# Optimization experiments

Measured on AMD Instinct MI355X. Metric: run time of the kernel, lower is better.

## Reference

```python
import jax, jax.numpy as jnp
import numpy as np

MAX_ITERS = 20
TOL = 1e-6
STEP = 1.0
EPS = 1e-7
CLIP = 1e-7


def _normalize(x, axis=-1):
    n = jnp.linalg.norm(x, axis=axis, keepdims=True)
    return x / jnp.maximum(n, 1e-12)


def _safe_acos(x):
    return jnp.arccos(jnp.clip(x, -1.0 + CLIP, 1.0 - CLIP))


def setup_inputs() -> dict:
    key = jax.random.key(0)
    NC, K, N, D = 1000, 8, 32, 128
    X_groups = jax.random.normal(key, (NC, K, N, D), dtype=jnp.float32)
    return {"X_groups": X_groups}


def reference(X_groups):
    # X_groups: (NC, K, N, D)
    NC, K, N, D = X_groups.shape
    X = X_groups.reshape(NC * K, N, D)
    Xn = _normalize(X)                      # (G, N, D) unit vectors
    mu = _normalize(jnp.mean(Xn, axis=1))   # (G, D) init mean

    done = jnp.array(False)
    for _ in range(MAX_ITERS):
        dots = jnp.einsum('gd,gnd->gn', mu, Xn)             # (G, N)
        theta = _safe_acos(dots)
        sin_t = jnp.maximum(jnp.sin(theta), EPS)
        diff = Xn - dots[..., None] * mu[:, None, :]        # (G, N, D)
        log_vecs = (theta / sin_t)[..., None] * diff        # log map
        v = jnp.mean(log_vecs, axis=1)                      # (G, D)
        v_norm = jnp.maximum(jnp.linalg.norm(v, axis=-1, keepdims=True), EPS)
        done = done | (jnp.max(v_norm) < TOL)               # global convergence (as in torch .item() check)
        v_step = STEP * v
        vs_norm = jnp.maximum(jnp.linalg.norm(v_step, axis=-1, keepdims=True), EPS)
        mu_new = jnp.cos(vs_norm) * mu + jnp.sin(vs_norm) * (v_step / vs_norm)  # exp map
        mu_new = _normalize(mu_new)
        mu = jnp.where(done, mu, mu_new)

    # calc_cluster_distance: features (G, N, D) @ means (G, D)
    sims = jnp.einsum('gnd,gd->gn', Xn, mu)
    sims = jnp.clip(sims, -1 + CLIP, 1 - CLIP)
    loss = jnp.mean(jnp.sum(jnp.arccos(sims) ** 2, axis=-1))
    return loss
```

## Files before the change

### kernel.cpp

```cpp
#include <hip/hip_runtime.h>
#include <stdint.h>

#define MAX_ITERS 20
#define EPSV 1e-7f
#define CLIPV 1e-7f
#define PI_F 3.14159265358979f
#define PIO2_F 1.57079632679490f

typedef __attribute__((ext_vector_type(8))) short short8;
typedef __attribute__((ext_vector_type(4))) float f4;

__device__ __forceinline__ f4 mfma_bf16(short8 a, short8 b, f4 c) {
    return __builtin_amdgcn_mfma_f32_16x16x32_bf16(a, b, c, 0, 0, 0);
}

__device__ __forceinline__ float rl(float v, int l) {
    return __int_as_float(__builtin_amdgcn_readlane(__float_as_int(v), l));
}

template <int CTRL>
__device__ __forceinline__ float dpp_add(float v) {
    int p = __builtin_amdgcn_update_dpp(0, __float_as_int(v), CTRL, 0xF, 0xF, true);
    return v + __int_as_float(p);
}
template <int CTRL>
__device__ __forceinline__ float dpp_mov(float v) {
    return __int_as_float(__builtin_amdgcn_update_dpp(0, __float_as_int(v), CTRL, 0xF, 0xF, true));
}

__device__ __forceinline__ float rowsum16(float v) {
    v = dpp_add<0xB1>(v);
    v = dpp_add<0x4E>(v);
    v = dpp_add<0x141>(v);
    v = dpp_add<0x140>(v);
    return v;
}

__device__ __forceinline__ float halfsum_rl(float v, bool hB) {
    v = rowsum16(v);
    float sA = rl(v, 0) + rl(v, 16);
    float sB = rl(v, 32) + rl(v, 48);
    return hB ? sB : sA;
}

__device__ __forceinline__ float halfsum_sw(float v) {
    v = rowsum16(v);
    int sw = __builtin_amdgcn_ds_swizzle(__float_as_int(v), 0x401F);
    return v + __int_as_float(sw);
}

__device__ __forceinline__ float fast_acos(float x) {
    float a = fabsf(x);
    bool big = a > 0.5f;
    float z = big ? 0.5f * (1.0f - a) : x * x;
    float s = big ? sqrtf(z) : x;
    float p = fmaf(z, fmaf(z, fmaf(z, fmaf(z, 4.2163199048e-2f, 2.4181311049e-2f),
                                   4.5470025998e-2f), 7.4953002686e-2f),
                   1.6666752422e-1f);
    float r = fmaf(s * z, p, s);
    float big_val = (x < 0.0f) ? (PI_F - 2.0f * r) : (2.0f * r);
    return big ? big_val : (PIO2_F - r);
}

__device__ __forceinline__ void cvt_hilo(const float* v, short8& hi, short8& lo) {
#pragma unroll
    for (int i = 0; i < 8; ++i) {
        float x = v[i];
        uint32_t u = __float_as_uint(x);
        float hf = __uint_as_float(u & 0xFFFF0000u);
        float lf = x - hf;
        hi[i] = (short)(u >> 16);
        lo[i] = (short)(__float_as_uint(lf) >> 16);
    }
}

#define WSTEPA(CTRL, GI) { curA = dpp_mov<CTRL>(curA); accA = fmaf(Grow2[GI], curA, accA); }
#define WSTEPB(CTRL, GI) { curB = dpp_mov<CTRL>(curB); accB = fmaf(Grow2[(GI) + 16], curB, accB); }

#define GLOAD_LDS16(srcp, ldsp)                                                   \
    __builtin_amdgcn_global_load_lds(                                             \
        (const __attribute__((address_space(1))) uint32_t*)(srcp),                \
        (__attribute__((address_space(3))) uint32_t*)(ldsp), 16, 0, 0)

__device__ __forceinline__ int gidx(int row, int j) {
    return row * 32 + ((((j >> 2) ^ (row & 7)) << 2) | (j & 3));
}

__global__ void __launch_bounds__(256, 4) karcher(const float* __restrict__ X,
                                                  float* __restrict__ ws,
                                                  int n_groups) {
    __shared__ float lds[4][2048];
    __shared__ float sInv[4][64];
    __shared__ float sPart[8];

    const int lane = threadIdx.x & 63;
    const int wid  = threadIdx.x >> 6;
    const int g0   = blockIdx.x * 8 + wid * 2;
    if (g0 >= n_groups) return;

    const int col  = lane & 15;
    const int quad = lane >> 4;

    float* slotA = lds[wid];
    float* slotB = lds[wid] + 1024;

    const int rrl = lane >> 3;
    const int g2l = lane & 7;
    auto stage = [&](const float* Xg, int kq, float* slot) {
#pragma unroll
        for (int i = 0; i < 4; ++i) {
            int rr  = i * 8 + rrl;
            int g2s = g2l ^ (rr & 7);
            GLOAD_LDS16(Xg + rr * 128 + kq * 32 + g2s * 4, slot + i * 256);
        }
    };

    const int x0 = col & 7;
    const int b0 = col * 32;
    const int b1 = (col + 16) * 32;
    f4 a00 = {0.f, 0.f, 0.f, 0.f}, a01 = a00, a10 = a00, a11 = a00;
    auto gramq = [&](const float* st) {
        int s0 = ((quad * 2 + 0) ^ x0) * 4;
        int s1 = ((quad * 2 + 1) ^ x0) * 4;
        float r0[8], r1[8];
        *(float4*)(r0)     = *(const float4*)(st + b0 + s0);
        *(float4*)(r0 + 4) = *(const float4*)(st + b0 + s1);
        *(float4*)(r1)     = *(const float4*)(st + b1 + s0);
        *(float4*)(r1 + 4) = *(const float4*)(st + b1 + s1);
        short8 H0, L0, H1, L1;
        cvt_hilo(r0, H0, L0);
        cvt_hilo(r1, H1, L1);
        a00 = mfma_bf16(H0, H0, a00);
        a00 = mfma_bf16(H0, L0, a00);
        a00 = mfma_bf16(L0, H0, a00);
        a01 = mfma_bf16(H0, H1, a01);
        a01 = mfma_bf16(H0, L1, a01);
        a01 = mfma_bf16(L0, H1, a01);
        a10 = mfma_bf16(H1, H0, a10);
        a10 = mfma_bf16(H1, L0, a10);
        a10 = mfma_bf16(L1, H0, a10);
        a11 = mfma_bf16(H1, H1, a11);
        a11 = mfma_bf16(H1, L1, a11);
        a11 = mfma_bf16(L1, H1, a11);
    };

    auto writeG = [&](float* Gs) {
#pragma unroll
        for (int i = 0; i < 4; ++i) {
            int rw = quad * 4 + i;
            Gs[gidx(rw,      col)]      = a00[i];
            Gs[gidx(rw,      col + 16)] = a01[i];
            Gs[gidx(rw + 16, col)]      = a10[i];
            Gs[gidx(rw + 16, col + 16)] = a11[i];
        }
    };

#define WAIT_VM0() do {                                   \
        asm volatile("s_waitcnt vmcnt(0)" ::: "memory");  \
        __builtin_amdgcn_sched_barrier(0);                \
    } while (0)

    {
        const float* Xg = X + (size_t)g0 * 4096;
        stage(Xg, 0, slotA);
        WAIT_VM0();
        gramq(slotA);
        stage(Xg, 1, slotB);
        WAIT_VM0();
        gramq(slotB);
        stage(Xg, 2, slotA);
        WAIT_VM0();
        gramq(slotA);
        stage(Xg, 3, slotB);
        WAIT_VM0();
        gramq(slotB);
        writeG(slotA);
    }
    {
        const float* Xg = X + (size_t)(g0 + 1) * 4096;
        a00 = {0.f, 0.f, 0.f, 0.f}; a01 = a00; a10 = a00; a11 = a00;
        stage(Xg, 0, slotB);
        WAIT_VM0();
        gramq(slotB);
        stage(Xg, 1, slotB);
        WAIT_VM0();
        gramq(slotB);
        stage(Xg, 2, slotB);
        WAIT_VM0();
        gramq(slotB);
        stage(Xg, 3, slotB);
        WAIT_VM0();
        gramq(slotB);
        writeG(slotB);
    }

    const int  half = lane >> 5;
    const bool hB   = half != 0;
    const int  r    = lane & 31;
    const float* Gh = lds[wid] + half * 1024;

    float inv = 1.0f / fmaxf(sqrtf(Gh[gidx(r, r)]), 1e-12f);
    sInv[wid][lane] = inv;
    const float* sI = sInv[wid] + half * 32;

    float Grow2[32];
#pragma unroll
    for (int gg = 0; gg < 32; ++gg) {
        int j = r ^ gg;
        Grow2[gg] = Gh[gidx(r, j)] * (inv * sI[j]);
    }

    float a = 1.0f / 32.0f;
    float ga;
    {
        float s0 = 0, s1 = 0, s2 = 0, s3 = 0;
#pragma unroll
        for (int gg = 0; gg < 8; ++gg) {
            s0 += Grow2[gg];
            s1 += Grow2[gg + 8];
            s2 += Grow2[gg + 16];
            s3 += Grow2[gg + 24];
        }
        ga = ((s0 + s1) + (s2 + s3)) * (1.0f / 32.0f);
        float n2   = halfsum_rl(a * ga, hB);
        float inv0 = 1.0f / fmaxf(sqrtf(n2), 1e-12f);
        a  *= inv0;
        ga *= inv0;
    }

    for (int it = 0; it < MAX_ITERS; ++it) {
        float x  = fminf(fmaxf(ga, -1.0f + CLIPV), 1.0f - CLIPV);
        float th = fast_acos(x);
        float st = fmaxf(sqrtf(fmaxf(1.0f - x * x, 0.0f)), EPSV);
        float w  = __fdividef(th, st);

        int w16i = __builtin_amdgcn_ds_swizzle(__float_as_int(w), 0x401F);
        float C = halfsum_sw(w * ga);

        float curA = w;
        float accA = Grow2[0] * curA;
        WSTEPA(0xB1, 1)   WSTEPA(0x4E, 3)   WSTEPA(0xB1, 2)   WSTEPA(0x141, 6)
        WSTEPA(0xB1, 7)   WSTEPA(0x4E, 5)   WSTEPA(0xB1, 4)   WSTEPA(0x140, 12)
        WSTEPA(0xB1, 13)  WSTEPA(0x4E, 15)  WSTEPA(0xB1, 14)  WSTEPA(0x141, 10)
        WSTEPA(0xB1, 11)  WSTEPA(0x4E, 9)   WSTEPA(0xB1, 8)

        float curB = __int_as_float(w16i);
        float accB = Grow2[16] * curB;
        WSTEPB(0xB1, 1)   WSTEPB(0x4E, 3)   WSTEPB(0xB1, 2)   WSTEPB(0x141, 6)
        WSTEPB(0xB1, 7)   WSTEPB(0x4E, 5)   WSTEPB(0xB1, 4)   WSTEPB(0x140, 12)
        WSTEPB(0xB1, 13)  WSTEPB(0x4E, 15)  WSTEPB(0xB1, 14)  WSTEPB(0x141, 10)
        WSTEPB(0xB1, 11)  WSTEPB(0x4E, 9)   WSTEPB(0xB1, 8)

        float gw   = accA + accB;
        float gb   = (gw - C * ga) * (1.0f / 32.0f);
        float beta = (w  - C * a ) * (1.0f / 32.0f);

        float vv = halfsum_rl(beta * gb, hB);
        float vs = fmaxf(sqrtf(fmaxf(vv, 0.0f)), EPSV);
        float cv = __cosf(vs);
        float sv = __fdividef(__sinf(vs), vs);
        a  = fmaf(sv, beta, cv * a);
        ga = fmaf(sv, gb, cv * ga);
        if (__all(vs < 1e-6f)) break;
    }

    float xf = fminf(fmaxf(ga, -1.0f + CLIPV), 1.0f - CLIPV);
    float t  = fast_acos(xf);
    float ls = halfsum_rl(t * t, hB);
    if (r == 0) sPart[wid * 2 + half] = ls;
    __syncthreads();
    if (threadIdx.x == 0) {
        float s = 0.f;
#pragma unroll
        for (int i = 0; i < 8; ++i) s += sPart[i];
        ws[blockIdx.x] = s;
    }
}

__global__ void __launch_bounds__(256) reduce_partials(const float* __restrict__ ws,
                                                       float* __restrict__ out,
                                                       int n, float scale) {
    __shared__ float sred[4];
    float s = 0.f;
    for (int i = threadIdx.x; i < n; i += 256) s += ws[i];
#pragma unroll
    for (int m = 32; m >= 1; m >>= 1) s += __shfl_xor(s, m, 64);
    const int lane = threadIdx.x & 63, wid = threadIdx.x >> 6;
    if (lane == 0) sred[wid] = s;
    __syncthreads();
    if (threadIdx.x == 0)
        out[0] = ((sred[0] + sred[1]) + (sred[2] + sred[3])) * scale;
}

extern "C" void kernel_launch(void* const* d_in, const int* in_sizes, int n_in,
                              void* d_out, int out_size, void* d_ws, size_t ws_size,
                              hipStream_t stream) {
    const float* X = (const float*)d_in[0];
    float* out = (float*)d_out;
    float* ws = (float*)d_ws;
    int n_groups = in_sizes[0] / (32 * 128);
    int blocks = (n_groups + 7) / 8;
    karcher<<<blocks, 256, 0, stream>>>(X, ws, n_groups);
    reduce_partials<<<1, 256, 0, stream>>>(ws, out, blocks, 1.0f / (float)n_groups);
}
```

Before: 211.1 us.

## Double-buffer global-to-LDS staging, shrink blocks, and split Gram-vector chain into four

```diff
diff --git a/kernel.cpp b/kernel.cpp
--- a/kernel.cpp
+++ b/kernel.cpp
@@ -26,6 +26,11 @@
 template <int CTRL>
 __device__ __forceinline__ float dpp_mov(float v) {
     return __int_as_float(__builtin_amdgcn_update_dpp(0, __float_as_int(v), CTRL, 0xF, 0xF, true));
+}
+
+template <int PAT>
+__device__ __forceinline__ float swz(float v) {
+    return __int_as_float(__builtin_amdgcn_ds_swizzle(__float_as_int(v), PAT));
 }
 
 __device__ __forceinline__ float rowsum16(float v) {
@@ -45,8 +50,7 @@
 
 __device__ __forceinline__ float halfsum_sw(float v) {
     v = rowsum16(v);
-    int sw = __builtin_amdgcn_ds_swizzle(__float_as_int(v), 0x401F);
-    return v + __int_as_float(sw);
+    return v + swz<0x401F>(v);
 }
 
 __device__ __forceinline__ float fast_acos(float x) {
@@ -74,35 +78,48 @@
     }
 }
 
-#define WSTEPA(CTRL, GI) { curA = dpp_mov<CTRL>(curA); accA = fmaf(Grow2[GI], curA, accA); }
-#define WSTEPB(CTRL, GI) { curB = dpp_mov<CTRL>(curB); accB = fmaf(Grow2[(GI) + 16], curB, accB); }
+#define CHAIN8(cur, acc, B)                                          \
+    acc = Grow2[B] * cur;                                            \
+    cur = dpp_mov<0xB1>(cur);  acc = fmaf(Grow2[(B)^1],  cur, acc);  \
+    cur = dpp_mov<0x4E>(cur);  acc = fmaf(Grow2[(B)^3],  cur, acc);  \
+    cur = dpp_mov<0xB1>(cur);  acc = fmaf(Grow2[(B)^2],  cur, acc);  \
+    cur = dpp_mov<0x128>(cur); acc = fmaf(Grow2[(B)^10], cur, acc);  \
+    cur = dpp_mov<0xB1>(cur);  acc = fmaf(Grow2[(B)^11], cur, acc);  \
+    cur = dpp_mov<0x4E>(cur);  acc = fmaf(Grow2[(B)^9],  cur, acc);  \
+    cur = dpp_mov<0xB1>(cur);  acc = fmaf(Grow2[(B)^8],  cur, acc);
 
 #define GLOAD_LDS16(srcp, ldsp)                                                   \
     __builtin_amdgcn_global_load_lds(                                             \
         (const __attribute__((address_space(1))) uint32_t*)(srcp),                \
         (__attribute__((address_space(3))) uint32_t*)(ldsp), 16, 0, 0)
 
+#define WAIT_VM(N) do {                                        \
+        asm volatile("s_waitcnt vmcnt(" #N ")" ::: "memory");  \
+        __builtin_amdgcn_sched_barrier(0);                     \
+    } while (0)
+
 __device__ __forceinline__ int gidx(int row, int j) {
     return row * 32 + ((((j >> 2) ^ (row & 7)) << 2) | (j & 3));
 }
 
-__global__ void __launch_bounds__(256, 4) karcher(const float* __restrict__ X,
+__global__ void __launch_bounds__(128, 4) karcher(const float* __restrict__ X,
                                                   float* __restrict__ ws,
                                                   int n_groups) {
-    __shared__ float lds[4][2048];
-    __shared__ float sInv[4][64];
-    __shared__ float sPart[8];
+    __shared__ float lds[2][3072];
+    __shared__ float sInv[2][64];
+    __shared__ float sPart[4];
 
     const int lane = threadIdx.x & 63;
     const int wid  = threadIdx.x >> 6;
-    const int g0   = blockIdx.x * 8 + wid * 2;
+    const int g0   = blockIdx.x * 4 + wid * 2;
     if (g0 >= n_groups) return;
 
     const int col  = lane & 15;
     const int quad = lane >> 4;
 
-    float* slotA = lds[wid];
-    float* slotB = lds[wid] + 1024;
+    float* slot0 = lds[wid];
+    float* slot1 = lds[wid] + 1024;
+    float* slot2 = lds[wid] + 2048;
 
     const int rrl = lane >> 3;
     const int g2l = lane & 7;
@@ -143,7 +160,6 @@
         a11 = mfma_bf16(H1, L1, a11);
         a11 = mfma_bf16(L1, H1, a11);
     };
-
     auto writeG = [&](float* Gs) {
 #pragma unroll
         for (int i = 0; i < 4; ++i) {
@@ -155,49 +171,29 @@
         }
     };
 
-#define WAIT_VM0() do {                                   \
-        asm volatile("s_waitcnt vmcnt(0)" ::: "memory");  \
-        __builtin_amdgcn_sched_barrier(0);                \
-    } while (0)
-
     {
-        const float* Xg = X + (size_t)g0 * 4096;
-        stage(Xg, 0, slotA);
-        WAIT_VM0();
-        gramq(slotA);
-        stage(Xg, 1, slotB);
-        WAIT_VM0();
-        gramq(slotB);
-        stage(Xg, 2, slotA);
-        WAIT_VM0();
-        gramq(slotA);
-        stage(Xg, 3, slotB);
-        WAIT_VM0();
-        gramq(slotB);
-        writeG(slotA);
-    }
-    {
-        const float* Xg = X + (size_t)(g0 + 1) * 4096;
+        const float* Xa = X + (size_t)g0 * 4096;
+        const float* Xb = X + (size_t)(g0 + 1) * 4096;
+        stage(Xa, 0, slot0);
+        stage(Xa, 1, slot1);
+        WAIT_VM(4);  gramq(slot0);  stage(Xa, 2, slot0);
+        WAIT_VM(4);  gramq(slot1);  stage(Xa, 3, slot1);
+        WAIT_VM(4);  gramq(slot0);  stage(Xb, 0, slot0);
+        WAIT_VM(4);  gramq(slot1);
+        writeG(slot2);
         a00 = {0.f, 0.f, 0.f, 0.f}; a01 = a00; a10 = a00; a11 = a00;
-        stage(Xg, 0, slotB);
-        WAIT_VM0();
-        gramq(slotB);
-        stage(Xg, 1, slotB);
-        WAIT_VM0();
-        gramq(slotB);
-        stage(Xg, 2, slotB);
-        WAIT_VM0();
-        gramq(slotB);
-        stage(Xg, 3, slotB);
-        WAIT_VM0();
-        gramq(slotB);
-        writeG(slotB);
+        stage(Xb, 1, slot1);
+        WAIT_VM(4);  gramq(slot0);  stage(Xb, 2, slot0);
+        WAIT_VM(4);  gramq(slot1);  stage(Xb, 3, slot1);
+        WAIT_VM(4);  gramq(slot0);
+        WAIT_VM(0);  gramq(slot1);
+        writeG(slot0);
     }
 
     const int  half = lane >> 5;
     const bool hB   = half != 0;
     const int  r    = lane & 31;
-    const float* Gh = lds[wid] + half * 1024;
+    const float* Gh = hB ? slot0 : slot2;
 
     float inv = 1.0f / fmaxf(sqrtf(Gh[gidx(r, r)]), 1e-12f);
     sInv[wid][lane] = inv;
@@ -234,24 +230,19 @@
         float st = fmaxf(sqrtf(fmaxf(1.0f - x * x, 0.0f)), EPSV);
         float w  = __fdividef(th, st);
 
-        int w16i = __builtin_amdgcn_ds_swizzle(__float_as_int(w), 0x401F);
+        float w4  = swz<0x101F>(w);
+        float w16 = swz<0x401F>(w);
+        float w20 = swz<0x501F>(w);
         float C = halfsum_sw(w * ga);
 
-        float curA = w;
-        float accA = Grow2[0] * curA;
-        WSTEPA(0xB1, 1)   WSTEPA(0x4E, 3)   WSTEPA(0xB1, 2)   WSTEPA(0x141, 6)
-        WSTEPA(0xB1, 7)   WSTEPA(0x4E, 5)   WSTEPA(0xB1, 4)   WSTEPA(0x140, 12)
-        WSTEPA(0xB1, 13)  WSTEPA(0x4E, 15)  WSTEPA(0xB1, 14)  WSTEPA(0x141, 10)
-        WSTEPA(0xB1, 11)  WSTEPA(0x4E, 9)   WSTEPA(0xB1, 8)
-
-        float curB = __int_as_float(w16i);
-        float accB = Grow2[16] * curB;
-        WSTEPB(0xB1, 1)   WSTEPB(0x4E, 3)   WSTEPB(0xB1, 2)   WSTEPB(0x141, 6)
-        WSTEPB(0xB1, 7)   WSTEPB(0x4E, 5)   WSTEPB(0xB1, 4)   WSTEPB(0x140, 12)
-        WSTEPB(0xB1, 13)  WSTEPB(0x4E, 15)  WSTEPB(0xB1, 14)  WSTEPB(0x141, 10)
-        WSTEPB(0xB1, 11)  WSTEPB(0x4E, 9)   WSTEPB(0xB1, 8)
-
-        float gw   = accA + accB;
+        float c0 = w,  c1 = w4, c2 = w16, c3 = w20;
+        float A0, A1, A2, A3;
+        CHAIN8(c0, A0, 0)
+        CHAIN8(c1, A1, 4)
+        CHAIN8(c2, A2, 16)
+        CHAIN8(c3, A3, 20)
+        float gw = (A0 + A1) + (A2 + A3);
+
         float gb   = (gw - C * ga) * (1.0f / 32.0f);
         float beta = (w  - C * a ) * (1.0f / 32.0f);
 
@@ -269,12 +260,8 @@
     float ls = halfsum_rl(t * t, hB);
     if (r == 0) sPart[wid * 2 + half] = ls;
     __syncthreads();
-    if (threadIdx.x == 0) {
-        float s = 0.f;
-#pragma unroll
-        for (int i = 0; i < 8; ++i) s += sPart[i];
-        ws[blockIdx.x] = s;
-    }
+    if (threadIdx.x == 0)
+        ws[blockIdx.x] = (sPart[0] + sPart[1]) + (sPart[2] + sPart[3]);
 }
 
 __global__ void __launch_bounds__(256) reduce_partials(const float* __restrict__ ws,
@@ -299,7 +286,7 @@
     float* out = (float*)d_out;
     float* ws = (float*)d_ws;
     int n_groups = in_sizes[0] / (32 * 128);
-    int blocks = (n_groups + 7) / 8;
-    karcher<<<blocks, 256, 0, stream>>>(X, ws, n_groups);
+    int blocks = (n_groups + 3) / 4;
+    karcher<<<blocks, 128, 0, stream>>>(X, ws, n_groups);
     reduce_partials<<<1, 256, 0, stream>>>(ws, out, blocks, 1.0f / (float)n_groups);
 }
```

After: 213.9 us. About the same (+1.3%).
